# Kernel optimization log

Measured on AMD Instinct MI355X. Metric: run time of the kernel, lower is better.

Reference implementation:

```python
import jax, jax.numpy as jnp
import numpy as np

B, T, O, N, M, H = 64, 128, 256, 65536, 64, 512
EPS = 1e-8


def setup_inputs() -> dict:
    key = jax.random.key(0)
    ks = jax.random.split(key, 8)
    x = jax.random.normal(ks[0], (B, T, O, 1), dtype=jnp.float32)
    # original: memory.uniform_(1e-05, 0.0001)
    memory0 = jax.random.uniform(ks[1], (N, M), dtype=jnp.float32, minval=1e-5, maxval=1e-4)
    eye = jnp.eye(B, N, dtype=jnp.float32)  # torch.eye(batch_size, N)
    h0 = jnp.zeros((B, H), dtype=jnp.float32)
    Wxh = jax.random.normal(ks[2], (O, H), dtype=jnp.float32) * 0.05
    Wrh = jax.random.normal(ks[3], (M, H), dtype=jnp.float32) * 0.1
    bh = jnp.zeros((H,), dtype=jnp.float32)
    Wo = jax.random.normal(ks[4], (H, O), dtype=jnp.float32) * 0.05
    bo = jnp.zeros((O,), dtype=jnp.float32)
    rW = jax.random.normal(ks[5], (H, M + 6), dtype=jnp.float32) * 0.05
    rb = jnp.zeros((M + 6,), dtype=jnp.float32)
    wW = jax.random.normal(ks[6], (H, 3 * M + 6), dtype=jnp.float32) * 0.05
    wb = jnp.zeros((3 * M + 6,), dtype=jnp.float32)
    return dict(x=x, memory0=memory0, wr=eye, ww=eye, h0=h0, Wxh=Wxh, Wrh=Wrh,
                bh=bh, Wo=Wo, bo=bo, rW=rW, rb=rb, wW=wW, wb=wb)


def _address(head_out, w_prev, mem):
    """Graves-2014 NTM addressing. head_out: (B, M+6) raw head projection."""
    k = jnp.tanh(head_out[:, :M])                          # key       (B, M)
    beta = jax.nn.softplus(head_out[:, M:M + 1])           # strength  (B, 1)
    g = jax.nn.sigmoid(head_out[:, M + 1:M + 2])           # gate      (B, 1)
    s = jax.nn.softmax(head_out[:, M + 2:M + 5], axis=-1)  # shift     (B, 3)
    gamma = 1.0 + jax.nn.softplus(head_out[:, M + 5:M + 6])  # sharpen (B, 1)
    kn = k / (jnp.linalg.norm(k, axis=-1, keepdims=True) + EPS)
    mn = mem / (jnp.linalg.norm(mem, axis=-1, keepdims=True) + EPS)
    wc = jax.nn.softmax(beta * (kn @ mn.T), axis=-1)       # content   (B, N)
    wg = g * wc + (1.0 - g) * w_prev                       # interpolate
    # circular shift conv over N with taps {-1, 0, +1}
    wt = (s[:, 0:1] * jnp.roll(wg, 1, axis=1)
          + s[:, 1:2] * wg
          + s[:, 2:3] * jnp.roll(wg, -1, axis=1))
    wp = (wt + EPS) ** gamma                               # sharpen
    return wp / jnp.sum(wp, axis=1, keepdims=True)


def reference(x, memory0, wr, ww, h0, Wxh, Wrh, bh, Wo, bo, rW, rb, wW, wb):
    xt = jnp.transpose(x, (1, 0, 2, 3)).reshape(T, B, O)  # time-major, flattened
    inv_b = 1.0 / B

    def step(carry, x_t):
        mem, h = carry
        # write head: address, then erase/add (memory shared across batch -> mean)
        wh = h @ wW + wb                                   # (B, 3M+6)
        w_w = _address(wh[:, :M + 6], ww, mem)             # (B, N)
        e = jax.nn.sigmoid(wh[:, M + 6:2 * M + 6])         # (B, M)
        a = jnp.tanh(wh[:, 2 * M + 6:3 * M + 6])           # (B, M)
        erase = jnp.einsum('bn,bm->nm', w_w, e) * inv_b    # (N, M)
        add = jnp.einsum('bn,bm->nm', w_w, a) * inv_b
        m_t = mem * (1.0 - erase) + add
        # read head
        rh = h @ rW + rb                                   # (B, M+6)
        w_r = _address(rh, wr, m_t)                        # (B, N)
        r_t = w_r @ m_t                                    # (B, M)
        # feedforward controller step + output
        h_new = jax.nn.relu(x_t @ Wxh + r_t @ Wrh + bh)    # (B, H)
        out = jax.nn.sigmoid(h_new @ Wo + bo)              # (B, O)
        return (m_t, h_new), out

    (_, _), outs = jax.lax.scan(step, (memory0, h0), xt)   # outs: (T, B, O)
    return jnp.transpose(outs, (1, 0, 2))                  # (B, T, O)
```

## Files before the change

### kernel.cpp

```cpp
#include <hip/hip_runtime.h>

#define NROWS 65536
#define BB 64
#define TT 128
#define OO 256
#define MM 64
#define HH 512
#define EPSF 1e-8f

__device__ __forceinline__ float wredsum(float v) {
#pragma unroll
  for (int o = 1; o < 64; o <<= 1) v += __shfl_xor(v, o, 64);
  return v;
}
__device__ __forceinline__ float sigm(float x) { return 1.f / (1.f + __expf(-x)); }
__device__ __forceinline__ float softplus_(float x) { return x > 20.f ? x : log1pf(__expf(x)); }

__global__ void __launch_bounds__(256) k_xpre(const float* __restrict__ x, const float* __restrict__ Wxh,
                                              const float* __restrict__ bh, float* __restrict__ Xpre) {
  __shared__ float xl[4][256];
  int tid = threadIdx.x;
#pragma unroll
  for (int i = 0; i < 4; ++i) {
    int pair = blockIdx.x * 4 + i;
    int t = pair >> 6, b = pair & 63;
    xl[i][tid] = x[((size_t)b * TT + t) * OO + tid];
  }
  __syncthreads();
  for (int u = 0; u < 2; ++u) {
    int hh = tid + u * 256;
    float a[4];
    float bv = bh[hh];
#pragma unroll
    for (int i = 0; i < 4; ++i) a[i] = bv;
    for (int o = 0; o < 256; ++o) {
      float wv = Wxh[(size_t)o * HH + hh];
#pragma unroll
      for (int i = 0; i < 4; ++i) a[i] += xl[i][o] * wv;
    }
#pragma unroll
    for (int i = 0; i < 4; ++i) {
      int pair = blockIdx.x * 4 + i;
      Xpre[(size_t)pair * HH + hh] = a[i];
    }
  }
}

__global__ void __launch_bounds__(256) k_w1(const float* __restrict__ msrc, const float* __restrict__ knw,
                                            const float* __restrict__ prmw, float* __restrict__ E,
                                            float* __restrict__ Swst, float* __restrict__ S2rst) {
  int tid = threadIdx.x, blk = blockIdx.x;
  int base = blk * 64;
  __shared__ float rows[4096];
  __shared__ float nrm[64];
  __shared__ float sred[256];
  if (blk == 0) {
    for (int i = tid; i < 32 * 64; i += 256) S2rst[i] = 0.f;
  }
  {
    const float4* s4 = (const float4*)(msrc + (size_t)base * 64);
    float4* d4 = (float4*)rows;
#pragma unroll
    for (int i = 0; i < 4; ++i) d4[tid + i * 256] = s4[tid + i * 256];
  }
  int l = tid & 63, w = tid >> 6;
  float4 kreg[16];
  {
    const float4* k4 = (const float4*)(knw + l * 64);
#pragma unroll
    for (int j = 0; j < 16; ++j) kreg[j] = k4[j];
  }
  float beta = prmw[l * 8 + 0];
  __syncthreads();
  for (int r = w * 16; r < w * 16 + 16; ++r) {
    float v = rows[r * 64 + l];
    float s = wredsum(v * v);
    if (l == 0) nrm[r] = sqrtf(s);
  }
  __syncthreads();
  float sacc = 0.f;
  for (int r = w * 16; r < w * 16 + 16; ++r) {
    const float4* row4 = (const float4*)(rows + r * 64);
    float dot = 0.f;
#pragma unroll
    for (int j = 0; j < 16; ++j) {
      float4 rv = row4[j], kv = kreg[j];
      dot += kv.x * rv.x + kv.y * rv.y + kv.z * rv.z + kv.w * rv.w;
    }
    float ev = __expf(beta * dot / (nrm[r] + EPSF) - beta);
    E[(size_t)(base + r) * 64 + l] = ev;
    sacc += ev;
  }
  sred[tid] = sacc;
  __syncthreads();
  if (tid < 64)
    atomicAdd(&Swst[(blk & 31) * 64 + tid], sred[tid] + sred[tid + 64] + sred[tid + 128] + sred[tid + 192]);
}

__global__ void __launch_bounds__(256) k_w2(const float* __restrict__ E, const float* __restrict__ prmw,
                                            const float* __restrict__ Swst, float* __restrict__ wpg,
                                            float* __restrict__ S2wst) {
  int tid = threadIdx.x, blk = blockIdx.x, base = blk * 64;
  __shared__ float Sw[64];
  __shared__ float sred[256];
  if (tid < 64) {
    float s = 0.f;
    for (int st = 0; st < 32; ++st) s += Swst[st * 64 + tid];
    Sw[tid] = s;
  }
  __syncthreads();
  int b = tid & 63, w = tid >> 6;
  float g = prmw[b * 8 + 1], gam = prmw[b * 8 + 2];
  float s0 = prmw[b * 8 + 3], s1 = prmw[b * 8 + 4], s2 = prmw[b * 8 + 5];
  float gi = g / Sw[b], gm1 = 1.f - g;
  float s2acc = 0.f;
  for (int i = 0; i < 16; ++i) {
    int n = base + w + i * 4;
    int nm = (n - 1) & (NROWS - 1), np = (n + 1) & (NROWS - 1);
    float wgm = gi * E[(size_t)nm * 64 + b] + (nm == b ? gm1 : 0.f);
    float wgc = gi * E[(size_t)n * 64 + b] + (n == b ? gm1 : 0.f);
    float wgp = gi * E[(size_t)np * 64 + b] + (np == b ? gm1 : 0.f);
    float wt = s0 * wgm + s1 * wgc + s2 * wgp;
    float wp = __powf(wt + EPSF, gam);
    wpg[(size_t)n * 64 + b] = wp;
    s2acc += wp;
  }
  sred[tid] = s2acc;
  __syncthreads();
  if (tid < 64)
    atomicAdd(&S2wst[(blk & 31) * 64 + tid], sred[tid] + sred[tid + 64] + sred[tid + 128] + sred[tid + 192]);
}

__global__ void __launch_bounds__(256) k_w3(const float* __restrict__ msrc, float* __restrict__ mdst,
                                            const float* __restrict__ wpg, const float* __restrict__ ea2,
                                            const float* __restrict__ knr, const float* __restrict__ prmr,
                                            const float* __restrict__ S2wst, float* __restrict__ E,
                                            float* __restrict__ Srst) {
  int tid = threadIdx.x, blk = blockIdx.x, base = blk * 64;
  __shared__ float2 ealds[4096];
  __shared__ float wlT[4 * 64 * 20];
  __shared__ float nrm[64];
  __shared__ float fb[64];
  __shared__ float sred[256];
  {
    const float4* s4 = (const float4*)ea2;
    float4* d4 = (float4*)ealds;
#pragma unroll
    for (int i = 0; i < 8; ++i) d4[tid + i * 256] = s4[tid + i * 256];
  }
  if (tid < 64) {
    float s = 0.f;
    for (int st = 0; st < 32; ++st) s += S2wst[st * 64 + tid];
    fb[tid] = 1.f / (64.f * s);
  }
  __syncthreads();
  int l = tid & 63, w = tid >> 6;
#pragma unroll
  for (int k = 0; k < 16; ++k) {
    float wv = wpg[(size_t)(base + w * 16 + k) * 64 + l] * fb[l];
    wlT[(w * 64 + l) * 20 + k] = wv;
  }
  __syncthreads();
  float er[16], ad[16];
#pragma unroll
  for (int k = 0; k < 16; ++k) { er[k] = 0.f; ad[k] = 0.f; }
  for (int b2 = 0; b2 < 64; ++b2) {
    float2 eav = ealds[b2 * 64 + l];
    const float4* wrow = (const float4*)(wlT + (w * 64 + b2) * 20);
    float4 q0 = wrow[0], q1 = wrow[1], q2 = wrow[2], q3 = wrow[3];
    float qa[16];
    qa[0] = q0.x; qa[1] = q0.y; qa[2] = q0.z; qa[3] = q0.w;
    qa[4] = q1.x; qa[5] = q1.y; qa[6] = q1.z; qa[7] = q1.w;
    qa[8] = q2.x; qa[9] = q2.y; qa[10] = q2.z; qa[11] = q2.w;
    qa[12] = q3.x; qa[13] = q3.y; qa[14] = q3.z; qa[15] = q3.w;
#pragma unroll
    for (int k = 0; k < 16; ++k) { er[k] += qa[k] * eav.x; ad[k] += qa[k] * eav.y; }
  }
#pragma unroll
  for (int k = 0; k < 16; ++k) {
    int r = w * 16 + k;
    size_t n = (size_t)(base + r);
    float mv = msrc[n * 64 + l];
    float nv = mv * (1.f - er[k]) + ad[k];
    mdst[n * 64 + l] = nv;
    float s = wredsum(nv * nv);
    if (l == 0) nrm[r] = sqrtf(s);
  }
  __syncthreads();
  float4 kreg[16];
  {
    const float4* k4 = (const float4*)(knr + l * 64);
#pragma unroll
    for (int j = 0; j < 16; ++j) kreg[j] = k4[j];
  }
  float beta_r = prmr[l * 8 + 0];
  float sacc = 0.f;
  for (int r = w * 16; r < w * 16 + 16; ++r) {
    const float4* row4 = (const float4*)(mdst + (size_t)(base + r) * 64);
    float dot = 0.f;
#pragma unroll
    for (int j = 0; j < 16; ++j) {
      float4 rv = row4[j], kv = kreg[j];
      dot += kv.x * rv.x + kv.y * rv.y + kv.z * rv.z + kv.w * rv.w;
    }
    float ev = __expf(beta_r * dot / (nrm[r] + EPSF) - beta_r);
    E[(size_t)(base + r) * 64 + l] = ev;
    sacc += ev;
  }
  sred[tid] = sacc;
  __syncthreads();
  if (tid < 64)
    atomicAdd(&Srst[(blk & 31) * 64 + tid], sred[tid] + sred[tid + 64] + sred[tid + 128] + sred[tid + 192]);
}

__global__ void __launch_bounds__(256) k_r2(const float* __restrict__ E, const float* __restrict__ mdst,
                                            const float* __restrict__ prmr, const float* __restrict__ Srst,
                                            float* __restrict__ part, float* __restrict__ S2rst) {
  int tid = threadIdx.x, blk = blockIdx.x, base = blk * 64;
  __shared__ float mt[4096];
  __shared__ float Sr[64];
  __shared__ float sred[256];
  __shared__ float racc[64 * 65];
  if (tid < 64) {
    float s = 0.f;
    for (int st = 0; st < 32; ++st) s += Srst[st * 64 + tid];
    Sr[tid] = s;
  }
  {
    const float4* s4 = (const float4*)(mdst + (size_t)base * 64);
    float4* d4 = (float4*)mt;
#pragma unroll
    for (int i = 0; i < 4; ++i) d4[tid + i * 256] = s4[tid + i * 256];
  }
  __syncthreads();
  int b = tid & 63, w = tid >> 6;
  float g = prmr[b * 8 + 1], gam = prmr[b * 8 + 2];
  float s0 = prmr[b * 8 + 3], s1 = prmr[b * 8 + 4], s2 = prmr[b * 8 + 5];
  float gi = g / Sr[b], gm1 = 1.f - g;
  float acc[64];
#pragma unroll
  for (int m = 0; m < 64; ++m) acc[m] = 0.f;
  float s2acc = 0.f;
  for (int i = 0; i < 16; ++i) {
    int r = w * 16 + i;
    int n = base + r;
    int nm = (n - 1) & (NROWS - 1), np = (n + 1) & (NROWS - 1);
    float wgm = gi * E[(size_t)nm * 64 + b] + (nm == b ? gm1 : 0.f);
    float wgc = gi * E[(size_t)n * 64 + b] + (n == b ? gm1 : 0.f);
    float wgp = gi * E[(size_t)np * 64 + b] + (np == b ? gm1 : 0.f);
    float wt = s0 * wgm + s1 * wgc + s2 * wgp;
    float wp = __powf(wt + EPSF, gam);
    s2acc += wp;
    const float4* row4 = (const float4*)(mt + r * 64);
#pragma unroll
    for (int m4 = 0; m4 < 16; ++m4) {
      float4 mv = row4[m4];
      acc[m4 * 4 + 0] += wp * mv.x;
      acc[m4 * 4 + 1] += wp * mv.y;
      acc[m4 * 4 + 2] += wp * mv.z;
      acc[m4 * 4 + 3] += wp * mv.w;
    }
  }
  sred[tid] = s2acc;
  __syncthreads();
  if (tid < 64)
    atomicAdd(&S2rst[(blk & 31) * 64 + tid], sred[tid] + sred[tid + 64] + sred[tid + 128] + sred[tid + 192]);
  if (w == 0) {
#pragma unroll
    for (int m = 0; m < 64; ++m) racc[b * 65 + m] = acc[m];
  }
  __syncthreads();
  for (int ww2 = 1; ww2 < 4; ++ww2) {
    if (w == ww2) {
#pragma unroll
      for (int m = 0; m < 64; ++m) racc[b * 65 + m] += acc[m];
    }
    __syncthreads();
  }
  for (int i = tid; i < 4096; i += 256) part[(size_t)blk * 4096 + i] = racc[(i >> 6) * 65 + (i & 63)];
}

__global__ void __launch_bounds__(256) k_rr(const float* __restrict__ part, float* __restrict__ part2) {
  __shared__ float red[256];
  int rb = blockIdx.x;
  int b = rb >> 2, quarter = rb & 3;
  int tid = threadIdx.x;
  int m = tid & 63, pq = tid >> 6;
  float acc = 0.f;
  for (int p = quarter * 256 + pq; p < quarter * 256 + 256; p += 4)
    acc += part[((size_t)p * 64 + b) * 64 + m];
  red[tid] = acc;
  __syncthreads();
  if (tid < 64)
    part2[(size_t)rb * 64 + tid] = red[tid] + red[tid + 64] + red[tid + 128] + red[tid + 192];
}

__global__ void __launch_bounds__(256) k_cp(int t, const float* __restrict__ h0,
                                            const float* __restrict__ Xpre, float* __restrict__ Hbuf,
                                            const float* __restrict__ part2, const float* __restrict__ S2rst,
                                            const float* __restrict__ Wrh, const float* __restrict__ wW,
                                            const float* __restrict__ wb, const float* __restrict__ rW,
                                            const float* __restrict__ rb, float* __restrict__ knw,
                                            float* __restrict__ knr, float* __restrict__ ea2,
                                            float* __restrict__ prmw, float* __restrict__ prmr,
                                            float* __restrict__ zst) {
  int b = blockIdx.x, tid = threadIdx.x;
  __shared__ float hl[512];
  __shared__ float proj[268];
  __shared__ float red[256];
  __shared__ float rt[64];
  __shared__ float s2r_sh;
  if (t >= 0) {
    float v = 0.f;
    if (tid < 32) v = S2rst[tid * 64 + b];
    red[tid] = v;
    __syncthreads();
    if (tid == 0) {
      float s = 0.f;
      for (int i = 0; i < 32; ++i) s += red[i];
      s2r_sh = s;
    }
    __syncthreads();
    int m = tid & 63, q = tid >> 6;
    red[tid] = part2[((size_t)b * 4 + q) * 64 + m];
    __syncthreads();
    if (tid < 64) rt[tid] = (red[tid] + red[tid + 64] + red[tid + 128] + red[tid + 192]) / s2r_sh;
    __syncthreads();
    for (int hh = tid; hh < 512; hh += 256) {
      float a = Xpre[((size_t)t * 64 + b) * HH + hh];
      for (int m2 = 0; m2 < 64; ++m2) a += rt[m2] * Wrh[(size_t)m2 * HH + hh];
      a = fmaxf(a, 0.f);
      Hbuf[((size_t)t * 64 + b) * HH + hh] = a;
      hl[hh] = a;
    }
  } else {
    for (int hh = tid; hh < 512; hh += 256) hl[hh] = h0[(size_t)b * HH + hh];
  }
  __syncthreads();
  if (b == 0) {
    for (int i = tid; i < 3 * 2048; i += 256) zst[i] = 0.f;
  }
  for (int idx = tid; idx < 268; idx += 256) {
    float a;
    if (idx < 198) {
      a = wb[idx];
      for (int hh = 0; hh < 512; ++hh) a += hl[hh] * wW[(size_t)hh * 198 + idx];
    } else {
      int jj = idx - 198;
      a = rb[jj];
      for (int hh = 0; hh < 512; ++hh) a += hl[hh] * rW[(size_t)hh * 70 + jj];
    }
    proj[idx] = a;
  }
  __syncthreads();
  int l = tid & 63, wv = tid >> 6;
  if (wv == 0) {
    float kv = tanhf(proj[l]);
    float s = wredsum(kv * kv);
    knw[b * 64 + l] = kv / (sqrtf(s) + EPSF);
  } else if (wv == 1) {
    float kv = tanhf(proj[198 + l]);
    float s = wredsum(kv * kv);
    knr[b * 64 + l] = kv / (sqrtf(s) + EPSF);
  } else if (wv == 2) {
    float ev = sigm(proj[70 + l]);
    float av = tanhf(proj[134 + l]);
    ((float2*)ea2)[b * 64 + l] = make_float2(ev, av);
  } else {
    if (l == 0) {
      float beta = softplus_(proj[64]);
      float g = sigm(proj[65]);
      float v0 = proj[66], v1 = proj[67], v2 = proj[68];
      float mx = fmaxf(v0, fmaxf(v1, v2));
      float e0 = __expf(v0 - mx), e1 = __expf(v1 - mx), e2 = __expf(v2 - mx);
      float is = 1.f / (e0 + e1 + e2);
      float gam = 1.f + softplus_(proj[69]);
      prmw[b * 8 + 0] = beta; prmw[b * 8 + 1] = g; prmw[b * 8 + 2] = gam;
      prmw[b * 8 + 3] = e0 * is; prmw[b * 8 + 4] = e1 * is; prmw[b * 8 + 5] = e2 * is;
    } else if (l == 1) {
      const int of = 198;
      float beta = softplus_(proj[of + 64]);
      float g = sigm(proj[of + 65]);
      float v0 = proj[of + 66], v1 = proj[of + 67], v2 = proj[of + 68];
      float mx = fmaxf(v0, fmaxf(v1, v2));
      float e0 = __expf(v0 - mx), e1 = __expf(v1 - mx), e2 = __expf(v2 - mx);
      float is = 1.f / (e0 + e1 + e2);
      float gam = 1.f + softplus_(proj[of + 69]);
      prmr[b * 8 + 0] = beta; prmr[b * 8 + 1] = g; prmr[b * 8 + 2] = gam;
      prmr[b * 8 + 3] = e0 * is; prmr[b * 8 + 4] = e1 * is; prmr[b * 8 + 5] = e2 * is;
    }
  }
}

__global__ void __launch_bounds__(256) k_out(const float* __restrict__ Hbuf, const float* __restrict__ Wo,
                                             const float* __restrict__ bo, float* __restrict__ out) {
  __shared__ float hl[4][512];
  int tid = threadIdx.x;
#pragma unroll
  for (int i = 0; i < 8; ++i) {
    int idx = tid + i * 256;
    hl[idx >> 9][idx & 511] = Hbuf[(size_t)blockIdx.x * 2048 + idx];
  }
  __syncthreads();
  float a[4];
  float bv = bo[tid];
#pragma unroll
  for (int i = 0; i < 4; ++i) a[i] = bv;
  for (int hh = 0; hh < 512; ++hh) {
    float wv = Wo[(size_t)hh * OO + tid];
#pragma unroll
    for (int i = 0; i < 4; ++i) a[i] += hl[i][hh] * wv;
  }
#pragma unroll
  for (int i = 0; i < 4; ++i) {
    int pair = blockIdx.x * 4 + i;
    int t = pair >> 6, b = pair & 63;
    out[((size_t)b * TT + t) * OO + tid] = 1.f / (1.f + __expf(-a[i]));
  }
}

extern "C" void kernel_launch(void* const* d_in, const int* in_sizes, int n_in,
                              void* d_out, int out_size, void* d_ws, size_t ws_size,
                              hipStream_t stream) {
  (void)in_sizes; (void)n_in; (void)out_size; (void)ws_size;
  const float* x    = (const float*)d_in[0];
  const float* mem0 = (const float*)d_in[1];
  const float* h0   = (const float*)d_in[4];
  const float* Wxh  = (const float*)d_in[5];
  const float* Wrh  = (const float*)d_in[6];
  const float* bh   = (const float*)d_in[7];
  const float* Wo   = (const float*)d_in[8];
  const float* bo   = (const float*)d_in[9];
  const float* rW   = (const float*)d_in[10];
  const float* rb   = (const float*)d_in[11];
  const float* wW   = (const float*)d_in[12];
  const float* wb   = (const float*)d_in[13];
  float* ws = (float*)d_ws;
  const size_t NM = (size_t)NROWS * MM;
  float* memA = ws;
  float* memB = memA + NM;
  float* E    = memB + NM;
  float* wpg  = E + NM;
  float* Xpre = wpg + NM;
  float* Hbuf = Xpre + NM;
  float* part = Hbuf + NM;
  float* part2 = part + NM;
  float* small = part2 + 16384;
  float* knw  = small;
  float* knr  = knw + 4096;
  float* ea2  = knr + 4096;
  float* prmw = ea2 + 8192;
  float* prmr = prmw + 512;
  float* Swst  = prmr + 512;
  float* S2wst = Swst + 2048;
  float* Srst  = S2wst + 2048;
  float* S2rst = Srst + 2048;

  hipMemcpyAsync(memA, mem0, NM * sizeof(float), hipMemcpyDeviceToDevice, stream);
  k_xpre<<<2048, 256, 0, stream>>>(x, Wxh, bh, Xpre);
  k_cp<<<64, 256, 0, stream>>>(-1, h0, Xpre, Hbuf, part2, S2rst, Wrh, wW, wb, rW, rb,
                               knw, knr, ea2, prmw, prmr, Swst);
  for (int t = 0; t < TT; ++t) {
    float* msrc = (t & 1) ? memB : memA;
    float* mdst = (t & 1) ? memA : memB;
    k_w1<<<1024, 256, 0, stream>>>(msrc, knw, prmw, E, Swst, S2rst);
    k_w2<<<1024, 256, 0, stream>>>(E, prmw, Swst, wpg, S2wst);
    k_w3<<<1024, 256, 0, stream>>>(msrc, mdst, wpg, ea2, knr, prmr, S2wst, E, Srst);
    k_r2<<<1024, 256, 0, stream>>>(E, mdst, prmr, Srst, part, S2rst);
    k_rr<<<256, 256, 0, stream>>>(part, part2);
    k_cp<<<64, 256, 0, stream>>>(t, h0, Xpre, Hbuf, part2, S2rst, Wrh, wW, wb, rW, rb,
                                 knw, knr, ea2, prmw, prmr, Swst);
  }
  k_out<<<2048, 256, 0, stream>>>(Hbuf, Wo, bo, (float*)d_out);
}
```

Before: 29.45 ms.

## Transpose key storage, fuse row norms into dot loop, stage E tiles in LDS

Normalized keys are now stored transposed so each lane loads its key column with coalesced reads. Row norms are computed inside the dot-product loop instead of a separate wave-reduction pass plus barrier. The shift-convolution kernels stage a 66-row halo tile of E in shared memory instead of reading each neighbor three times from global. The controller kernel now runs 512 threads so each hidden unit and projection gets one thread. This trades more registers (64-float key arrays) and extra LDS for fewer global loads and fewer syncs, which may lower occupancy.

Result: faster. 27.03 ms (-8.2%).

```diff
diff --git a/kernel.cpp b/kernel.cpp
--- a/kernel.cpp
+++ b/kernel.cpp
@@ -46,13 +46,12 @@
   }
 }
 
-__global__ void __launch_bounds__(256) k_w1(const float* __restrict__ msrc, const float* __restrict__ knw,
+__global__ void __launch_bounds__(256) k_w1(const float* __restrict__ msrc, const float* __restrict__ knwT,
                                             const float* __restrict__ prmw, float* __restrict__ E,
                                             float* __restrict__ Swst, float* __restrict__ S2rst) {
   int tid = threadIdx.x, blk = blockIdx.x;
   int base = blk * 64;
   __shared__ float rows[4096];
-  __shared__ float nrm[64];
   __shared__ float sred[256];
   if (blk == 0) {
     for (int i = tid; i < 32 * 64; i += 256) S2rst[i] = 0.f;
@@ -64,30 +63,22 @@
     for (int i = 0; i < 4; ++i) d4[tid + i * 256] = s4[tid + i * 256];
   }
   int l = tid & 63, w = tid >> 6;
-  float4 kreg[16];
-  {
-    const float4* k4 = (const float4*)(knw + l * 64);
-#pragma unroll
-    for (int j = 0; j < 16; ++j) kreg[j] = k4[j];
-  }
+  float kr[64];
+#pragma unroll
+  for (int j = 0; j < 64; ++j) kr[j] = knwT[j * 64 + l];
   float beta = prmw[l * 8 + 0];
-  __syncthreads();
-  for (int r = w * 16; r < w * 16 + 16; ++r) {
-    float v = rows[r * 64 + l];
-    float s = wredsum(v * v);
-    if (l == 0) nrm[r] = sqrtf(s);
-  }
   __syncthreads();
   float sacc = 0.f;
   for (int r = w * 16; r < w * 16 + 16; ++r) {
     const float4* row4 = (const float4*)(rows + r * 64);
-    float dot = 0.f;
+    float dot = 0.f, nsq = 0.f;
 #pragma unroll
     for (int j = 0; j < 16; ++j) {
-      float4 rv = row4[j], kv = kreg[j];
-      dot += kv.x * rv.x + kv.y * rv.y + kv.z * rv.z + kv.w * rv.w;
-    }
-    float ev = __expf(beta * dot / (nrm[r] + EPSF) - beta);
+      float4 rv = row4[j];
+      dot += kr[j * 4] * rv.x + kr[j * 4 + 1] * rv.y + kr[j * 4 + 2] * rv.z + kr[j * 4 + 3] * rv.w;
+      nsq += rv.x * rv.x + rv.y * rv.y + rv.z * rv.z + rv.w * rv.w;
+    }
+    float ev = __expf(beta * dot / (sqrtf(nsq) + EPSF) - beta);
     E[(size_t)(base + r) * 64 + l] = ev;
     sacc += ev;
   }
@@ -101,6 +92,7 @@
                                             const float* __restrict__ Swst, float* __restrict__ wpg,
                                             float* __restrict__ S2wst) {
   int tid = threadIdx.x, blk = blockIdx.x, base = blk * 64;
+  __shared__ float EL[66 * 64];
   __shared__ float Sw[64];
   __shared__ float sred[256];
   if (tid < 64) {
@@ -108,6 +100,10 @@
     for (int st = 0; st < 32; ++st) s += Swst[st * 64 + tid];
     Sw[tid] = s;
   }
+  for (int i = tid; i < 66 * 64; i += 256) {
+    int rr = i >> 6, b2 = i & 63;
+    EL[i] = E[(size_t)((base - 1 + rr) & (NROWS - 1)) * 64 + b2];
+  }
   __syncthreads();
   int b = tid & 63, w = tid >> 6;
   float g = prmw[b * 8 + 1], gam = prmw[b * 8 + 2];
@@ -115,11 +111,12 @@
   float gi = g / Sw[b], gm1 = 1.f - g;
   float s2acc = 0.f;
   for (int i = 0; i < 16; ++i) {
-    int n = base + w + i * 4;
+    int ln = w + i * 4;
+    int n = base + ln;
     int nm = (n - 1) & (NROWS - 1), np = (n + 1) & (NROWS - 1);
-    float wgm = gi * E[(size_t)nm * 64 + b] + (nm == b ? gm1 : 0.f);
-    float wgc = gi * E[(size_t)n * 64 + b] + (n == b ? gm1 : 0.f);
-    float wgp = gi * E[(size_t)np * 64 + b] + (np == b ? gm1 : 0.f);
+    float wgm = gi * EL[ln * 64 + b] + (nm == b ? gm1 : 0.f);
+    float wgc = gi * EL[(ln + 1) * 64 + b] + (n == b ? gm1 : 0.f);
+    float wgp = gi * EL[(ln + 2) * 64 + b] + (np == b ? gm1 : 0.f);
     float wt = s0 * wgm + s1 * wgc + s2 * wgp;
     float wp = __powf(wt + EPSF, gam);
     wpg[(size_t)n * 64 + b] = wp;
@@ -133,13 +130,12 @@
 
 __global__ void __launch_bounds__(256) k_w3(const float* __restrict__ msrc, float* __restrict__ mdst,
                                             const float* __restrict__ wpg, const float* __restrict__ ea2,
-                                            const float* __restrict__ knr, const float* __restrict__ prmr,
+                                            const float* __restrict__ knrT, const float* __restrict__ prmr,
                                             const float* __restrict__ S2wst, float* __restrict__ E,
                                             float* __restrict__ Srst) {
   int tid = threadIdx.x, blk = blockIdx.x, base = blk * 64;
   __shared__ float2 ealds[4096];
   __shared__ float wlT[4 * 64 * 20];
-  __shared__ float nrm[64];
   __shared__ float fb[64];
   __shared__ float sred[256];
   {
@@ -181,29 +177,24 @@
     int r = w * 16 + k;
     size_t n = (size_t)(base + r);
     float mv = msrc[n * 64 + l];
-    float nv = mv * (1.f - er[k]) + ad[k];
-    mdst[n * 64 + l] = nv;
-    float s = wredsum(nv * nv);
-    if (l == 0) nrm[r] = sqrtf(s);
-  }
-  __syncthreads();
-  float4 kreg[16];
-  {
-    const float4* k4 = (const float4*)(knr + l * 64);
-#pragma unroll
-    for (int j = 0; j < 16; ++j) kreg[j] = k4[j];
-  }
+    mdst[n * 64 + l] = mv * (1.f - er[k]) + ad[k];
+  }
+  __syncthreads();
+  float kr[64];
+#pragma unroll
+  for (int j = 0; j < 64; ++j) kr[j] = knrT[j * 64 + l];
   float beta_r = prmr[l * 8 + 0];
   float sacc = 0.f;
   for (int r = w * 16; r < w * 16 + 16; ++r) {
     const float4* row4 = (const float4*)(mdst + (size_t)(base + r) * 64);
-    float dot = 0.f;
+    float dot = 0.f, nsq = 0.f;
 #pragma unroll
     for (int j = 0; j < 16; ++j) {
-      float4 rv = row4[j], kv = kreg[j];
-      dot += kv.x * rv.x + kv.y * rv.y + kv.z * rv.z + kv.w * rv.w;
-    }
-    float ev = __expf(beta_r * dot / (nrm[r] + EPSF) - beta_r);
+      float4 rv = row4[j];
+      dot += kr[j * 4] * rv.x + kr[j * 4 + 1] * rv.y + kr[j * 4 + 2] * rv.z + kr[j * 4 + 3] * rv.w;
+      nsq += rv.x * rv.x + rv.y * rv.y + rv.z * rv.z + rv.w * rv.w;
+    }
+    float ev = __expf(beta_r * dot / (sqrtf(nsq) + EPSF) - beta_r);
     E[(size_t)(base + r) * 64 + l] = ev;
     sacc += ev;
   }
@@ -218,6 +209,7 @@
                                             float* __restrict__ part, float* __restrict__ S2rst) {
   int tid = threadIdx.x, blk = blockIdx.x, base = blk * 64;
   __shared__ float mt[4096];
+  __shared__ float EL[66 * 64];
   __shared__ float Sr[64];
   __shared__ float sred[256];
   __shared__ float racc[64 * 65];
@@ -232,6 +224,10 @@
 #pragma unroll
     for (int i = 0; i < 4; ++i) d4[tid + i * 256] = s4[tid + i * 256];
   }
+  for (int i = tid; i < 66 * 64; i += 256) {
+    int rr = i >> 6, b2 = i & 63;
+    EL[i] = E[(size_t)((base - 1 + rr) & (NROWS - 1)) * 64 + b2];
+  }
   __syncthreads();
   int b = tid & 63, w = tid >> 6;
   float g = prmr[b * 8 + 1], gam = prmr[b * 8 + 2];
@@ -245,9 +241,9 @@
     int r = w * 16 + i;
     int n = base + r;
     int nm = (n - 1) & (NROWS - 1), np = (n + 1) & (NROWS - 1);
-    float wgm = gi * E[(size_t)nm * 64 + b] + (nm == b ? gm1 : 0.f);
-    float wgc = gi * E[(size_t)n * 64 + b] + (n == b ? gm1 : 0.f);
-    float wgp = gi * E[(size_t)np * 64 + b] + (np == b ? gm1 : 0.f);
+    float wgm = gi * EL[r * 64 + b] + (nm == b ? gm1 : 0.f);
+    float wgc = gi * EL[(r + 1) * 64 + b] + (n == b ? gm1 : 0.f);
+    float wgp = gi * EL[(r + 2) * 64 + b] + (np == b ? gm1 : 0.f);
     float wt = s0 * wgm + s1 * wgc + s2 * wgp;
     float wp = __powf(wt + EPSF, gam);
     s2acc += wp;
@@ -295,25 +291,25 @@
     part2[(size_t)rb * 64 + tid] = red[tid] + red[tid + 64] + red[tid + 128] + red[tid + 192];
 }
 
-__global__ void __launch_bounds__(256) k_cp(int t, const float* __restrict__ h0,
+__global__ void __launch_bounds__(512) k_cp(int t, const float* __restrict__ h0,
                                             const float* __restrict__ Xpre, float* __restrict__ Hbuf,
                                             const float* __restrict__ part2, const float* __restrict__ S2rst,
                                             const float* __restrict__ Wrh, const float* __restrict__ wW,
                                             const float* __restrict__ wb, const float* __restrict__ rW,
-                                            const float* __restrict__ rb, float* __restrict__ knw,
-                                            float* __restrict__ knr, float* __restrict__ ea2,
+                                            const float* __restrict__ rb, float* __restrict__ knwT,
+                                            float* __restrict__ knrT, float* __restrict__ ea2,
                                             float* __restrict__ prmw, float* __restrict__ prmr,
                                             float* __restrict__ zst) {
   int b = blockIdx.x, tid = threadIdx.x;
   __shared__ float hl[512];
   __shared__ float proj[268];
-  __shared__ float red[256];
+  __shared__ float red[512];
   __shared__ float rt[64];
   __shared__ float s2r_sh;
   if (t >= 0) {
     float v = 0.f;
     if (tid < 32) v = S2rst[tid * 64 + b];
-    red[tid] = v;
+    if (tid < 64) red[tid] = v;
     __syncthreads();
     if (tid == 0) {
       float s = 0.f;
@@ -321,12 +317,15 @@
       s2r_sh = s;
     }
     __syncthreads();
-    int m = tid & 63, q = tid >> 6;
-    red[tid] = part2[((size_t)b * 4 + q) * 64 + m];
+    if (tid < 256) {
+      int m = tid & 63, q = tid >> 6;
+      red[tid] = part2[((size_t)b * 4 + q) * 64 + m];
+    }
     __syncthreads();
     if (tid < 64) rt[tid] = (red[tid] + red[tid + 64] + red[tid + 128] + red[tid + 192]) / s2r_sh;
     __syncthreads();
-    for (int hh = tid; hh < 512; hh += 256) {
+    {
+      int hh = tid;
       float a = Xpre[((size_t)t * 64 + b) * HH + hh];
       for (int m2 = 0; m2 < 64; ++m2) a += rt[m2] * Wrh[(size_t)m2 * HH + hh];
       a = fmaxf(a, 0.f);
@@ -334,13 +333,14 @@
       hl[hh] = a;
     }
   } else {
-    for (int hh = tid; hh < 512; hh += 256) hl[hh] = h0[(size_t)b * HH + hh];
+    hl[tid] = h0[(size_t)b * HH + tid];
   }
   __syncthreads();
   if (b == 0) {
-    for (int i = tid; i < 3 * 2048; i += 256) zst[i] = 0.f;
-  }
-  for (int idx = tid; idx < 268; idx += 256) {
+    for (int i = tid; i < 3 * 2048; i += 512) zst[i] = 0.f;
+  }
+  if (tid < 268) {
+    int idx = tid;
     float a;
     if (idx < 198) {
       a = wb[idx];
@@ -357,16 +357,16 @@
   if (wv == 0) {
     float kv = tanhf(proj[l]);
     float s = wredsum(kv * kv);
-    knw[b * 64 + l] = kv / (sqrtf(s) + EPSF);
+    knwT[l * 64 + b] = kv / (sqrtf(s) + EPSF);
   } else if (wv == 1) {
     float kv = tanhf(proj[198 + l]);
     float s = wredsum(kv * kv);
-    knr[b * 64 + l] = kv / (sqrtf(s) + EPSF);
+    knrT[l * 64 + b] = kv / (sqrtf(s) + EPSF);
   } else if (wv == 2) {
     float ev = sigm(proj[70 + l]);
     float av = tanhf(proj[134 + l]);
     ((float2*)ea2)[b * 64 + l] = make_float2(ev, av);
-  } else {
+  } else if (wv == 3) {
     if (l == 0) {
       float beta = softplus_(proj[64]);
       float g = sigm(proj[65]);
@@ -446,9 +446,9 @@
   float* part = Hbuf + NM;
   float* part2 = part + NM;
   float* small = part2 + 16384;
-  float* knw  = small;
-  float* knr  = knw + 4096;
-  float* ea2  = knr + 4096;
+  float* knwT = small;
+  float* knrT = knwT + 4096;
+  float* ea2  = knrT + 4096;
   float* prmw = ea2 + 8192;
   float* prmr = prmw + 512;
   float* Swst  = prmr + 512;
@@ -458,18 +458,18 @@
 
   hipMemcpyAsync(memA, mem0, NM * sizeof(float), hipMemcpyDeviceToDevice, stream);
   k_xpre<<<2048, 256, 0, stream>>>(x, Wxh, bh, Xpre);
-  k_cp<<<64, 256, 0, stream>>>(-1, h0, Xpre, Hbuf, part2, S2rst, Wrh, wW, wb, rW, rb,
-                               knw, knr, ea2, prmw, prmr, Swst);
+  k_cp<<<64, 512, 0, stream>>>(-1, h0, Xpre, Hbuf, part2, S2rst, Wrh, wW, wb, rW, rb,
+                               knwT, knrT, ea2, prmw, prmr, Swst);
   for (int t = 0; t < TT; ++t) {
     float* msrc = (t & 1) ? memB : memA;
     float* mdst = (t & 1) ? memA : memB;
-    k_w1<<<1024, 256, 0, stream>>>(msrc, knw, prmw, E, Swst, S2rst);
+    k_w1<<<1024, 256, 0, stream>>>(msrc, knwT, prmw, E, Swst, S2rst);
     k_w2<<<1024, 256, 0, stream>>>(E, prmw, Swst, wpg, S2wst);
-    k_w3<<<1024, 256, 0, stream>>>(msrc, mdst, wpg, ea2, knr, prmr, S2wst, E, Srst);
+    k_w3<<<1024, 256, 0, stream>>>(msrc, mdst, wpg, ea2, knrT, prmr, S2wst, E, Srst);
     k_r2<<<1024, 256, 0, stream>>>(E, mdst, prmr, Srst, part, S2rst);
     k_rr<<<256, 256, 0, stream>>>(part, part2);
-    k_cp<<<64, 256, 0, stream>>>(t, h0, Xpre, Hbuf, part2, S2rst, Wrh, wW, wb, rW, rb,
-                                 knw, knr, ea2, prmw, prmr, Swst);
+    k_cp<<<64, 512, 0, stream>>>(t, h0, Xpre, Hbuf, part2, S2rst, Wrh, wW, wb, rW, rb,
+                                 knwT, knrT, ea2, prmw, prmr, Swst);
   }
   k_out<<<2048, 256, 0, stream>>>(Hbuf, Wo, bo, (float*)d_out);
 }
```
